# Kernel tuning notes

Measured on AMD Instinct MI355X. Metric: run time of the kernel, lower is better.

## Reference

```python
import jax, jax.numpy as jnp
import numpy as np

B = 64        # graphs per batch
N0 = 131072   # total nodes (2048 per graph)
E = 1048576   # total edges (within-graph)
H = 128       # hidden_size
C = 7         # class_num (input feature dim)
EPS = 1e-5


def setup_inputs() -> dict:
    key = jax.random.key(0)
    ks = jax.random.split(key, 16)
    n0 = N0 // B
    x = jax.random.normal(ks[0], (N0, C), dtype=jnp.float32)
    # within-graph random edges: edge e belongs to graph e // (E//B)
    g = jnp.repeat(jnp.arange(B, dtype=jnp.int32), E // B)
    row = jax.random.randint(ks[1], (E,), 0, n0, dtype=jnp.int32) + g * n0
    col = jax.random.randint(ks[2], (E,), 0, n0, dtype=jnp.int32) + g * n0
    edge_index = jnp.stack([row, col], axis=0)
    batch = jnp.repeat(jnp.arange(B, dtype=jnp.int32), n0)
    s = 0.05
    params = dict(
        Wc1=jax.random.normal(ks[3], (C, H), jnp.float32) * s,     # conv1 weight
        Wc=jax.random.normal(ks[4], (3, H, H), jnp.float32) * s,   # conv2-4 weights
        bc=jax.random.normal(ks[5], (4, H), jnp.float32) * s,      # conv biases
        Wf=jax.random.normal(ks[6], (4, H, H), jnp.float32) * s,   # fc weights
        bf=jax.random.normal(ks[7], (4, H), jnp.float32) * s,      # fc biases
        bn_g=jnp.ones((4, H), jnp.float32),                        # BN gamma
        bn_b=jnp.zeros((4, H), jnp.float32),                       # BN beta
        Ws1=jax.random.normal(ks[8], (4, H, 1), jnp.float32) * s,  # SAG GraphConv root weight
        Ws2=jax.random.normal(ks[9], (4, H, 1), jnp.float32) * s,  # SAG GraphConv neighbor weight
        bs=jax.random.normal(ks[10], (4, 1), jnp.float32) * s,     # SAG GraphConv bias
    )
    return dict(x=x, edge_index=edge_index, batch=batch, **params)


def _gcn_conv(x, W, b, row, col, m, N):
    # PyG GCNConv with self loops: out_i = sum_{j->i} h_j / sqrt(d_i d_j) + h_i / d_i + b
    h = x @ W
    deg = jax.ops.segment_sum(m, col, num_segments=N) + 1.0  # +1 for self loop
    dis = jax.lax.rsqrt(deg)
    norm = dis[row] * dis[col] * m  # masked-out edges contribute 0
    agg = jax.ops.segment_sum(h[row] * norm[:, None], col, num_segments=N)
    return agg + h * (dis * dis)[:, None] + b


def _sag_score(x, W1, W2, b, row, col, m, N):
    # GraphConv(H, 1, aggr='add'): score_i = W1^T x_i + W2^T sum_{j->i} x_j + b
    nbr = jax.ops.segment_sum(x[row] * m[:, None], col, num_segments=N)
    return (x @ W1 + nbr @ W2 + b).reshape(-1)


def _bn(x, g, b):
    mu = jnp.mean(x, axis=0)
    var = jnp.mean((x - mu) ** 2, axis=0)  # biased, matches torch BN training
    return (x - mu) * jax.lax.rsqrt(var + EPS) * g + b


def reference(x, edge_index, batch, Wc1, Wc, bc, Wf, bf, bn_g, bn_b, Ws1, Ws2, bs):
    row, col = edge_index[0], edge_index[1]
    m = jnp.ones(row.shape, x.dtype)  # edge validity mask (static-size edge list)
    n = x.shape[0] // B               # nodes per graph (equal-size graphs)
    for i in range(4):
        N = B * n
        W = Wc1 if i == 0 else Wc[i - 1]
        h = _gcn_conv(x, W, bc[i], row, col, m, N)
        h = jax.nn.relu(h @ Wf[i] + bf[i])
        h = _bn(h, bn_g[i], bn_b[i])
        # SAGPooling(ratio=0.5): per-graph top-k by GraphConv score, x *= tanh(score)
        score = _sag_score(h, Ws1[i], Ws2[i], bs[i], row, col, m, N)
        k = n // 2
        _, idx = jax.lax.top_k(score.reshape(B, n), k)  # [B, k] per-graph indices
        perm = (idx + jnp.arange(B, dtype=idx.dtype)[:, None] * n).reshape(-1)
        x = h[perm] * jnp.tanh(score[perm])[:, None]
        # re-index edges; mask edges touching removed nodes
        inv = jnp.full((N,), -1, dtype=row.dtype).at[perm].set(
            jnp.arange(B * k, dtype=row.dtype))
        nr, nc = inv[row], inv[col]
        valid = (nr >= 0) & (nc >= 0)
        m = m * valid.astype(m.dtype)
        row = jnp.where(valid, nr, 0)
        col = jnp.where(valid, nc, 0)
        n = k
    # global_mean_pool over block-structured batch -> [B, H]
    return x.reshape(B, n, -1).mean(axis=1)
```

## Files before the change

### kernel.cpp

```cpp
#include <hip/hip_runtime.h>
#include <cstdint>

#define HB 128
#define NB 64
#define NE 1048576
#define SLAB 16384
#define XP 132

typedef float v2f __attribute__((ext_vector_type(2)));

__global__ __launch_bounds__(256) void init_edges_k(const int* __restrict__ ei,
    int* __restrict__ row, int* __restrict__ col, int* __restrict__ gcnt0, int E) {
  int e = blockIdx.x * blockDim.x + threadIdx.x;
  if (e < E) { row[e] = ei[e]; col[e] = ei[E + e]; }
  if (blockIdx.x == 0 && threadIdx.x < NB) gcnt0[threadIdx.x] = SLAB;
}

__global__ __launch_bounds__(256) void conv_fc0_k(const float* __restrict__ aggx,
    const float* __restrict__ Wc1, const float* __restrict__ bc0,
    const float* __restrict__ Wf, const float* __restrict__ bf0,
    float* __restrict__ out, int N, float* __restrict__ stat) {
  __shared__ float lt[64][128];
  __shared__ float laggx[64][8];
  __shared__ float lwc1[7 * 128];
  float2 (*red)[128] = (float2(*)[128])lt;
  int tid = threadIdx.x;
  int tx = tid & 31, ty = tid >> 5;
  long rowbase = (long)blockIdx.x * 64;
  for (int i = tid; i < 7 * 32; i += 256)
    ((float4*)lwc1)[i] = ((const float4*)Wc1)[i];
  if (tid < 128) {
    int lr = tid >> 1, lq = (tid & 1) * 4;
    *(float4*)&laggx[lr][lq] = *(const float4*)(aggx + (rowbase + lr) * 8 + lq);
  }
  __syncthreads();
  float4 tacc[8];
  float4 bcv = ((const float4*)bc0)[tx];
  #pragma unroll
  for (int r = 0; r < 8; ++r) tacc[r] = bcv;
  #pragma unroll
  for (int k = 0; k < 7; ++k) {
    float4 wv = ((float4*)lwc1)[k * 32 + tx];
    #pragma unroll
    for (int r = 0; r < 8; ++r) {
      float xv = laggx[ty + 8 * r][k];
      tacc[r].x += xv * wv.x; tacc[r].y += xv * wv.y;
      tacc[r].z += xv * wv.z; tacc[r].w += xv * wv.w;
    }
  }
  #pragma unroll
  for (int r = 0; r < 8; ++r)
    *(float4*)&lt[ty + 8 * r][4 * tx] = tacc[r];
  __syncthreads();
  v2f acc2[16];
  #pragma unroll
  for (int r = 0; r < 16; ++r) acc2[r] = (v2f){0.f, 0.f};
  for (int kc = 0; kc < 16; ++kc) {
    float4 wreg[8];
    #pragma unroll
    for (int k = 0; k < 8; ++k)
      wreg[k] = *(const float4*)(Wf + (size_t)(kc * 8 + k) * HB + 4 * tx);
    #pragma unroll
    for (int kk = 0; kk < 8; kk += 4) {
      float4 xreg[8];
      #pragma unroll
      for (int r = 0; r < 8; ++r)
        xreg[r] = *(const float4*)&lt[ty + 8 * r][kc * 8 + kk];
      #pragma unroll
      for (int k2 = 0; k2 < 4; ++k2) {
        float4 wv = wreg[kk + k2];
        v2f wlo = {wv.x, wv.y}, whi = {wv.z, wv.w};
        #pragma unroll
        for (int r = 0; r < 8; ++r) {
          float xv = ((const float*)&xreg[r])[k2];
          v2f xvv = {xv, xv};
          acc2[2 * r]     += xvv * wlo;
          acc2[2 * r + 1] += xvv * whi;
        }
      }
    }
  }
  float4 bv = ((const float4*)bf0)[tx];
  float4 psum = make_float4(0.f, 0.f, 0.f, 0.f);
  float4 psq  = make_float4(0.f, 0.f, 0.f, 0.f);
  __syncthreads();
  #pragma unroll
  for (int r = 0; r < 8; ++r) {
    float4 v;
    v.x = fmaxf(acc2[2 * r].x + bv.x, 0.f);
    v.y = fmaxf(acc2[2 * r].y + bv.y, 0.f);
    v.z = fmaxf(acc2[2 * r + 1].x + bv.z, 0.f);
    v.w = fmaxf(acc2[2 * r + 1].y + bv.w, 0.f);
    psum.x += v.x; psum.y += v.y; psum.z += v.z; psum.w += v.w;
    psq.x += v.x * v.x; psq.y += v.y * v.y;
    psq.z += v.z * v.z; psq.w += v.w * v.w;
    *(float4*)(out + (size_t)(rowbase + ty + 8 * r) * HB + 4 * tx) = v;
  }
  red[ty][4 * tx + 0] = make_float2(psum.x, psq.x);
  red[ty][4 * tx + 1] = make_float2(psum.y, psq.y);
  red[ty][4 * tx + 2] = make_float2(psum.z, psq.z);
  red[ty][4 * tx + 3] = make_float2(psum.w, psq.w);
  __syncthreads();
  if (tid < 128) {
    float s = 0.f, q = 0.f;
    #pragma unroll
    for (int t = 0; t < 8; ++t) { s += red[t][tid].x; q += red[t][tid].y; }
    float* st = stat + ((blockIdx.x & 7) << 8);
    atomicAdd(&st[tid], s);
    atomicAdd(&st[128 + tid], q);
  }
}

__global__ __launch_bounds__(256) void conv_fc_k(const float* __restrict__ Ap,
    const float* __restrict__ bnsc, const int* __restrict__ sel,
    const float* __restrict__ scale, const int* __restrict__ srowA,
    const float* __restrict__ snorm2, const int* __restrict__ off,
    const int* __restrict__ offe, const float* __restrict__ dis,
    const float* __restrict__ Wc, const float* __restrict__ bc0,
    const float* __restrict__ Wf, const float* __restrict__ bf0,
    float* __restrict__ out, int N, float* __restrict__ stat) {
  __shared__ float buf[64][XP];
  float2 (*red)[128] = (float2(*)[128])buf;
  int tid = threadIdx.x;
  int tx = tid & 31, ty = tid >> 5;
  long cpx = gridDim.x >> 3;
  long bb = ((long)blockIdx.x & 7) * cpx + ((long)blockIdx.x >> 3);
  long rowbase = bb * 64;
  {
    int r = tid >> 2;
    int chq = (tid & 3) * 32;
    int node = rowbase + r;
    int e0 = off[node], e1 = offe[node];
    float dv = dis[node];
    float4 acc[8];
    float ssum;
    {
      float sc = scale[node] * dv * dv;
      ssum = sc;
      const float* xr = Ap + (size_t)sel[node] * HB + chq;
      #pragma unroll
      for (int q = 0; q < 8; ++q) {
        float4 v = *(const float4*)(xr + 4 * q);
        acc[q].x = v.x * sc; acc[q].y = v.y * sc;
        acc[q].z = v.z * sc; acc[q].w = v.w * sc;
      }
    }
    for (int j = e0; j < e1; ++j) {
      float sc = snorm2[j];
      const float* xr = Ap + (size_t)srowA[j] * HB + chq;
      ssum += sc;
      #pragma unroll
      for (int q = 0; q < 8; ++q) {
        float4 v = *(const float4*)(xr + 4 * q);
        acc[q].x += v.x * sc; acc[q].y += v.y * sc;
        acc[q].z += v.z * sc; acc[q].w += v.w * sc;
      }
    }
    #pragma unroll
    for (int q = 0; q < 8; ++q) {
      float4 a  = *(const float4*)(bnsc + chq + 4 * q);
      float4 b8 = *(const float4*)(bnsc + 128 + chq + 4 * q);
      float4 o;
      o.x = a.x * acc[q].x + b8.x * ssum;
      o.y = a.y * acc[q].y + b8.y * ssum;
      o.z = a.z * acc[q].z + b8.z * ssum;
      o.w = a.w * acc[q].w + b8.w * ssum;
      *(float4*)&buf[r][chq + 4 * q] = o;
    }
  }
  __syncthreads();
  {
    float4 bcv = ((const float4*)bc0)[tx];
    v2f acc2[16];
    #pragma unroll
    for (int r = 0; r < 8; ++r) {
      acc2[2 * r]     = (v2f){bcv.x, bcv.y};
      acc2[2 * r + 1] = (v2f){bcv.z, bcv.w};
    }
    for (int kc = 0; kc < 16; ++kc) {
      float4 wreg[8];
      #pragma unroll
      for (int k = 0; k < 8; ++k)
        wreg[k] = *(const float4*)(Wc + (size_t)(kc * 8 + k) * HB + 4 * tx);
      #pragma unroll
      for (int kk = 0; kk < 8; kk += 4) {
        float4 xreg[8];
        #pragma unroll
        for (int r = 0; r < 8; ++r)
          xreg[r] = *(const float4*)&buf[ty + 8 * r][kc * 8 + kk];
        #pragma unroll
        for (int k2 = 0; k2 < 4; ++k2) {
          float4 wv = wreg[kk + k2];
          v2f wlo = {wv.x, wv.y}, whi = {wv.z, wv.w};
          #pragma unroll
          for (int r = 0; r < 8; ++r) {
            float xv = ((const float*)&xreg[r])[k2];
            v2f xvv = {xv, xv};
            acc2[2 * r]     += xvv * wlo;
            acc2[2 * r + 1] += xvv * whi;
          }
        }
      }
    }
    __syncthreads();
    #pragma unroll
    for (int r = 0; r < 8; ++r) {
      float4 v;
      v.x = acc2[2 * r].x;     v.y = acc2[2 * r].y;
      v.z = acc2[2 * r + 1].x; v.w = acc2[2 * r + 1].y;
      *(float4*)&buf[ty + 8 * r][4 * tx] = v;
    }
  }
  __syncthreads();
  v2f acc2[16];
  #pragma unroll
  for (int r = 0; r < 16; ++r) acc2[r] = (v2f){0.f, 0.f};
  for (int kc = 0; kc < 16; ++kc) {
    float4 wreg[8];
    #pragma unroll
    for (int k = 0; k < 8; ++k)
      wreg[k] = *(const float4*)(Wf + (size_t)(kc * 8 + k) * HB + 4 * tx);
    #pragma unroll
    for (int kk = 0; kk < 8; kk += 4) {
      float4 xreg[8];
      #pragma unroll
      for (int r = 0; r < 8; ++r)
        xreg[r] = *(const float4*)&buf[ty + 8 * r][kc * 8 + kk];
      #pragma unroll
      for (int k2 = 0; k2 < 4; ++k2) {
        float4 wv = wreg[kk + k2];
        v2f wlo = {wv.x, wv.y}, whi = {wv.z, wv.w};
        #pragma unroll
        for (int r = 0; r < 8; ++r) {
          float xv = ((const float*)&xreg[r])[k2];
          v2f xvv = {xv, xv};
          acc2[2 * r]     += xvv * wlo;
          acc2[2 * r + 1] += xvv * whi;
        }
      }
    }
  }
  float4 bv = ((const float4*)bf0)[tx];
  float4 psum = make_float4(0.f, 0.f, 0.f, 0.f);
  float4 psq  = make_float4(0.f, 0.f, 0.f, 0.f);
  __syncthreads();
  #pragma unroll
  for (int r = 0; r < 8; ++r) {
    float4 v;
    v.x = fmaxf(acc2[2 * r].x + bv.x, 0.f);
    v.y = fmaxf(acc2[2 * r].y + bv.y, 0.f);
    v.z = fmaxf(acc2[2 * r + 1].x + bv.z, 0.f);
    v.w = fmaxf(acc2[2 * r + 1].y + bv.w, 0.f);
    psum.x += v.x; psum.y += v.y; psum.z += v.z; psum.w += v.w;
    psq.x += v.x * v.x; psq.y += v.y * v.y;
    psq.z += v.z * v.z; psq.w += v.w * v.w;
    *(float4*)(out + (size_t)(rowbase + ty + 8 * r) * HB + 4 * tx) = v;
  }
  red[ty][4 * tx + 0] = make_float2(psum.x, psq.x);
  red[ty][4 * tx + 1] = make_float2(psum.y, psq.y);
  red[ty][4 * tx + 2] = make_float2(psum.z, psq.z);
  red[ty][4 * tx + 3] = make_float2(psum.w, psq.w);
  __syncthreads();
  if (tid < 128) {
    float s = 0.f, q = 0.f;
    #pragma unroll
    for (int t = 0; t < 8; ++t) { s += red[t][tid].x; q += red[t][tid].y; }
    float* st = stat + (((int)blockIdx.x & 7) << 8);
    atomicAdd(&st[tid], s);
    atomicAdd(&st[128 + tid], q);
  }
}

__global__ __launch_bounds__(1024) void csr_build_k(const int* __restrict__ row,
    const int* __restrict__ col, const int* __restrict__ gcnt,
    const int* __restrict__ sel, const float* __restrict__ scale,
    float* __restrict__ dis, int* __restrict__ off, int* __restrict__ offe,
    int* __restrict__ srow, int* __restrict__ srowA,
    float* __restrict__ snorm, int n) {
  extern __shared__ int lds[];
  int* ldeg = lds;
  int* lsa  = lds + n;
  int* lsb  = lds + 2 * n;
  float* ldis = (float*)(lds + 3 * n);
  int g = blockIdx.x, tid = threadIdx.x;
  int e0 = g * SLAB, e1 = e0 + gcnt[g];
  int base = g * n;
  for (int i = tid; i < n; i += 1024) ldeg[i] = 0;
  __syncthreads();
  for (int e = e0 + tid; e < e1; e += 1024) atomicAdd(&ldeg[col[e] - base], 1);
  __syncthreads();
  for (int i = tid; i < n; i += 1024) {
    int d = ldeg[i];
    ldis[i] = rsqrtf((float)d + 1.f);
    lsa[i] = d;
  }
  __syncthreads();
  int* src = lsa; int* dst = lsb;
  for (int o = 1; o < n; o <<= 1) {
    for (int i = tid; i < n; i += 1024) dst[i] = src[i] + ((i >= o) ? src[i - o] : 0);
    __syncthreads();
    int* t = src; src = dst; dst = t;
  }
  for (int i = tid; i < n; i += 1024) {
    int d = ldeg[i];
    int ex = src[i] - d;
    off[base + i]  = e0 + ex;
    offe[base + i] = e0 + ex + d;
    ldeg[i] = ex;
    dis[base + i] = ldis[i];
  }
  __syncthreads();
  for (int e = e0 + tid; e < e1; e += 1024) {
    int r = row[e], c = col[e];
    int lc = c - base;
    int p = e0 + atomicAdd(&ldeg[lc], 1);
    srow[p] = r;
    float nm = ldis[r - base] * ldis[lc];
    if (sel) { srowA[p] = sel[r]; snorm[p] = nm * scale[r]; }
    else     { srowA[p] = r;      snorm[p] = nm; }
  }
}

__global__ __launch_bounds__(256) void agg7_k(const float* __restrict__ x,
    const int* __restrict__ srow, const float* __restrict__ snorm,
    const int* __restrict__ off, const int* __restrict__ offe,
    const float* __restrict__ dis, float* __restrict__ aggx, int N) {
  int cpx = gridDim.x >> 3;
  int b = blockIdx.x;
  int bid = (b & 7) * cpx + (b >> 3);
  int gid = bid * 256 + threadIdx.x;
  int node = gid >> 3, c = gid & 7;
  if (node >= N) return;
  float acc = 0.f;
  if (c < 7) {
    int s = off[node], e = offe[node];
    for (int j = s; j < e; ++j) acc += x[(size_t)srow[j] * 7 + c] * snorm[j];
    float d = dis[node];
    acc += x[(size_t)node * 7 + c] * d * d;
  }
  aggx[(size_t)node * 8 + c] = acc;
}

__global__ __launch_bounds__(128) void bnfin_k(const float* __restrict__ stat8,
    const float* __restrict__ g, const float* __restrict__ b,
    float* __restrict__ sc, int N) {
  int c = threadIdx.x;
  if (c < 128) {
    float s = 0.f, q = 0.f;
    #pragma unroll
    for (int sh = 0; sh < 8; ++sh) {
      s += stat8[sh * 256 + c];
      q += stat8[sh * 256 + 128 + c];
    }
    float mu = s / N;
    float var = q / N - mu * mu;
    float a = g[c] * rsqrtf(var + 1e-5f);
    sc[c] = a;
    sc[128 + c] = b[c] - mu * a;
  }
}

__global__ __launch_bounds__(256) void score_prep_k(const float* __restrict__ h,
    const float* __restrict__ sc, const float* __restrict__ w1,
    const float* __restrict__ w2, float* __restrict__ selfs,
    float* __restrict__ t2, int N) {
  int gid = blockIdx.x * blockDim.x + threadIdx.x;
  int node = gid >> 6;
  if (node >= N) return;
  int lane = gid & 63, c = lane * 2;
  float2 v = *(const float2*)(h + (size_t)node * HB + c);
  v.x = v.x * sc[c] + sc[128 + c];
  v.y = v.y * sc[c + 1] + sc[128 + c + 1];
  float s1 = v.x * w1[c] + v.y * w1[c + 1];
  float s2 = v.x * w2[c] + v.y * w2[c + 1];
  #pragma unroll
  for (int off = 32; off > 0; off >>= 1) {
    s1 += __shfl_xor(s1, off);
    s2 += __shfl_xor(s2, off);
  }
  if (lane == 0) { selfs[node] = s1; t2[node] = s2; }
}

__global__ __launch_bounds__(256) void score_k(const float* __restrict__ selfs,
    const float* __restrict__ t2, const int* __restrict__ srow,
    const int* __restrict__ off, const int* __restrict__ offe,
    const float* __restrict__ bs, float* __restrict__ score, int N) {
  int i = blockIdx.x * blockDim.x + threadIdx.x;
  if (i >= N) return;
  float s = selfs[i] + bs[0];
  int e0 = off[i], e1 = offe[i];
  for (int j = e0; j < e1; ++j) s += t2[srow[j]];
  score[i] = s;
}

__global__ __launch_bounds__(256) void rank_topk_k(const float* __restrict__ score,
    int* __restrict__ inv, int* __restrict__ sel, float* __restrict__ scale,
    int n, int k, int bpg) {
  extern __shared__ float ls[];
  int g = blockIdx.x / bpg, sub = blockIdx.x % bpg;
  int tid = threadIdx.x;
  const float* sg = score + (size_t)g * n;
  for (int i = tid; i < n; i += 256) ls[i] = sg[i];
  __syncthreads();
  int i0 = sub * 256 + tid;
  float s0 = ls[i0];
  int r0 = 0;
  for (int jb = 0; jb < n; jb += 4) {
    float4 v = *(const float4*)(ls + jb);
    r0 += (v.x > s0) || (v.x == s0 && (jb + 0) < i0);
    r0 += (v.y > s0) || (v.y == s0 && (jb + 1) < i0);
    r0 += (v.z > s0) || (v.z == s0 && (jb + 2) < i0);
    r0 += (v.w > s0) || (v.w == s0 && (jb + 3) < i0);
  }
  if (r0 < k) {
    inv[(size_t)g * n + i0] = g * k + r0;
    sel[(size_t)g * k + r0] = g * n + i0;
    scale[(size_t)g * k + r0] = tanhf(s0);
  } else inv[(size_t)g * n + i0] = -1;
}

__global__ __launch_bounds__(256) void gather_x_k(const float* __restrict__ h,
    const float* __restrict__ bnsc, const int* __restrict__ sel,
    const float* __restrict__ scale, float* __restrict__ xout, int M) {
  int gid = blockIdx.x * blockDim.x + threadIdx.x;
  int r = gid >> 5;
  if (r >= M) return;
  int ch = (gid & 31) * 4;
  int old = sel[r];
  float sc = scale[r];
  float4 v = *(const float4*)(h + (size_t)old * HB + ch);
  float4 a = *(const float4*)(bnsc + ch);
  float4 b = *(const float4*)(bnsc + 128 + ch);
  v.x = (v.x * a.x + b.x) * sc; v.y = (v.y * a.y + b.y) * sc;
  v.z = (v.z * a.z + b.z) * sc; v.w = (v.w * a.w + b.w) * sc;
  *(float4*)(xout + (size_t)r * HB + ch) = v;
}

__global__ __launch_bounds__(256) void cmp_k(const int* __restrict__ row,
    const int* __restrict__ col, const int* __restrict__ inv,
    const int* __restrict__ gcntCur, int* __restrict__ nrow,
    int* __restrict__ ncol, int* __restrict__ gcntNxt) {
  int g = blockIdx.x >> 6;
  int eloc = ((blockIdx.x & 63) << 8) + threadIdx.x;
  int cnt = gcntCur[g];
  if (((blockIdx.x & 63) << 8) >= cnt) return;
  long e = (long)g * SLAB + eloc;
  bool valid = false; int nr = 0, nc = 0;
  if (eloc < cnt) {
    nr = inv[row[e]]; nc = inv[col[e]];
    valid = (nr >= 0) && (nc >= 0);
  }
  unsigned long long mask = __ballot(valid);
  int lane = threadIdx.x & 63, wid = threadIdx.x >> 6;
  __shared__ int ws[4];
  __shared__ int base;
  if (lane == 0) ws[wid] = __popcll(mask);
  __syncthreads();
  if (threadIdx.x == 0) {
    int a = ws[0], b = ws[1], c2 = ws[2], d = ws[3];
    int tot = a + b + c2 + d;
    base = tot ? atomicAdd(&gcntNxt[g], tot) : 0;
    ws[0] = 0; ws[1] = a; ws[2] = a + b; ws[3] = a + b + c2;
  }
  __syncthreads();
  if (valid) {
    unsigned long long lt = ((unsigned long long)1 << lane) - 1;
    long o = (long)g * SLAB + base + ws[wid] + (int)__popcll(mask & lt);
    nrow[o] = nr;
    ncol[o] = nc;
  }
}

__global__ __launch_bounds__(128) void pool_k(const float* __restrict__ x,
    float* __restrict__ out, int n) {
  int g = blockIdx.x, c = threadIdx.x;
  float s = 0.f;
  for (int r = 0; r < n; ++r) s += x[((size_t)g * n + r) * HB + c];
  out[g * HB + c] = s / n;
}

extern "C" void kernel_launch(void* const* d_in, const int* in_sizes, int n_in,
                              void* d_out, int out_size, void* d_ws, size_t ws_size,
                              hipStream_t stream) {
  const float* x_in = (const float*)d_in[0];
  const int*   ei   = (const int*)d_in[1];
  const float* Wc1  = (const float*)d_in[3];
  const float* Wc   = (const float*)d_in[4];
  const float* bc   = (const float*)d_in[5];
  const float* Wf   = (const float*)d_in[6];
  const float* bf   = (const float*)d_in[7];
  const float* bng  = (const float*)d_in[8];
  const float* bnb  = (const float*)d_in[9];
  const float* Ws1  = (const float*)d_in[10];
  const float* Ws2  = (const float*)d_in[11];
  const float* bs   = (const float*)d_in[12];

  const int N0 = 131072, E = NE;
  char* p = (char*)d_ws;
  auto alloc = [&](size_t bytes) -> char* {
    char* r = p; p += (bytes + 255) & ~(size_t)255; return r;
  };
  float* A    = (float*)alloc((size_t)N0 * HB * 4);
  float* Bb   = (float*)alloc((size_t)N0 * HB * 4);
  float* Cc   = (float*)alloc((size_t)(N0 / 2) * HB * 4);
  float* aggx = (float*)alloc((size_t)N0 * 8 * 4);
  int*   rowA = (int*)alloc((size_t)E * 4);
  int*   colA = (int*)alloc((size_t)E * 4);
  int*   rowB = (int*)alloc((size_t)E * 4);
  int*   colB = (int*)alloc((size_t)E * 4);
  int*   srowA= (int*)alloc((size_t)E * 4);
  float* dis  = (float*)alloc((size_t)N0 * 4);
  float* selfs= (float*)alloc((size_t)N0 * 4);
  float* t2v  = (float*)alloc((size_t)N0 * 4);
  float* score= (float*)alloc((size_t)N0 * 4);
  int*   inv  = (int*)alloc((size_t)N0 * 4);
  int*   off  = (int*)alloc((size_t)N0 * 4);
  int*   offe = (int*)alloc((size_t)N0 * 4);
  int*   sel  = (int*)alloc((size_t)(N0 / 2) * 4);
  float* scale= (float*)alloc((size_t)(N0 / 2) * 4);
  int*   gcntL= (int*)alloc(4 * NB * 4);
  float* stat8= (float*)alloc(4 * 8 * 256 * 4);
  float* bnsc = (float*)alloc(256 * 4);

  hipMemsetAsync(stat8, 0, 4 * 8 * 256 * 4, stream);
  hipMemsetAsync(gcntL, 0, 4 * NB * 4, stream);

  init_edges_k<<<E / 256, 256, 0, stream>>>(ei, rowA, colA, gcntL, E);

  int* rowCur = rowA; int* colCur = colA;
  int* rowNxt = rowB; int* colNxt = colB;

  int n = 2048;
  for (int i = 0; i < 4; ++i) {
    int N = NB * n, khalf = n >> 1;
    float* statL = stat8 + (size_t)i * 8 * 256;
    const float* Xin  = (i == 2) ? Bb : A;
    float*       Xout = (i == 0 || i == 2) ? A : Bb;
    int*   srow  = rowNxt;
    float* snorm = (float*)colNxt;
    csr_build_k<<<NB, 1024, (size_t)16 * n, stream>>>(
        rowCur, colCur, gcntL + i * NB, (i == 0) ? nullptr : sel,
        (i == 0) ? nullptr : scale, dis, off, offe, srow, srowA, snorm, n);
    if (i == 0) {
      agg7_k<<<N / 32, 256, 0, stream>>>(x_in, srow, snorm, off, offe, dis, aggx, N);
      conv_fc0_k<<<N / 64, 256, 0, stream>>>(aggx, Wc1, bc, Wf, bf, Xout, N, statL);
    } else {
      conv_fc_k<<<N / 64, 256, 0, stream>>>(
          Xin, bnsc, sel, scale, srowA, snorm, off, offe, dis,
          Wc + (size_t)(i - 1) * HB * HB, bc + (size_t)i * HB,
          Wf + (size_t)i * HB * HB, bf + (size_t)i * HB, Xout, N, statL);
    }
    bnfin_k<<<1, 128, 0, stream>>>(statL, bng + (size_t)i * HB, bnb + (size_t)i * HB, bnsc, N);
    score_prep_k<<<N / 4, 256, 0, stream>>>(
        Xout, bnsc, Ws1 + (size_t)i * HB, Ws2 + (size_t)i * HB, selfs, t2v, N);
    score_k<<<(N + 255) / 256, 256, 0, stream>>>(
        selfs, t2v, srow, off, offe, bs + i, score, N);
    int bpg = n / 256;
    rank_topk_k<<<NB * bpg, 256, (size_t)n * 4, stream>>>(
        score, inv, sel, scale, n, khalf, bpg);
    if (i < 3) {
      cmp_k<<<NB * 64, 256, 0, stream>>>(rowCur, colCur, inv, gcntL + i * NB,
                                         rowNxt, colNxt, gcntL + (i + 1) * NB);
      int* t;
      t = rowCur; rowCur = rowNxt; rowNxt = t;
      t = colCur; colCur = colNxt; colNxt = t;
    } else {
      gather_x_k<<<(NB * khalf) / 8, 256, 0, stream>>>(
          Xout, bnsc, sel, scale, Cc, NB * khalf);
    }
    n = khalf;
  }
  pool_k<<<NB, 128, 0, stream>>>(Cc, (float*)d_out, n);
}
```

Measured before the change: 601.6 us.

## Split fused gather-aggregate and dense FC kernel into two separate kernels

Splits conv_fc_k into gatherx_k, which does the irregular neighbor gather and normalization and writes the aggregated features to a new xagg buffer, and fc2_k, which loads xagg and runs the two dense matmuls plus the BN statistics. The aim is to stop the latency-bound gather from stalling the compute-heavy GEMM in the same block, so each kernel can reach its own occupancy and scheduling. The cost is an extra global round trip of an N×128 float buffer and one more launch per layer.

```diff
diff --git a/kernel.cpp b/kernel.cpp
--- a/kernel.cpp
+++ b/kernel.cpp
@@ -111,11 +111,60 @@
   }
 }
 
-__global__ __launch_bounds__(256) void conv_fc_k(const float* __restrict__ Ap,
+__global__ __launch_bounds__(256) void gatherx_k(const float* __restrict__ Ap,
     const float* __restrict__ bnsc, const int* __restrict__ sel,
     const float* __restrict__ scale, const int* __restrict__ srowA,
     const float* __restrict__ snorm2, const int* __restrict__ off,
     const int* __restrict__ offe, const float* __restrict__ dis,
+    float* __restrict__ xagg, int N) {
+  int cpx = gridDim.x >> 3;
+  int b = blockIdx.x;
+  int bid = (b & 7) * cpx + (b >> 3);
+  int gid = bid * 256 + threadIdx.x;
+  int node = gid >> 2;
+  if (node >= N) return;
+  int chq = (gid & 3) * 32;
+  int e0 = off[node], e1 = offe[node];
+  float dv = dis[node];
+  float4 acc[8];
+  float ssum;
+  {
+    float sc = scale[node] * dv * dv;
+    ssum = sc;
+    const float* xr = Ap + (size_t)sel[node] * HB + chq;
+    #pragma unroll
+    for (int q = 0; q < 8; ++q) {
+      float4 v = *(const float4*)(xr + 4 * q);
+      acc[q].x = v.x * sc; acc[q].y = v.y * sc;
+      acc[q].z = v.z * sc; acc[q].w = v.w * sc;
+    }
+  }
+  for (int j = e0; j < e1; ++j) {
+    float sc = snorm2[j];
+    const float* xr = Ap + (size_t)srowA[j] * HB + chq;
+    ssum += sc;
+    #pragma unroll
+    for (int q = 0; q < 8; ++q) {
+      float4 v = *(const float4*)(xr + 4 * q);
+      acc[q].x += v.x * sc; acc[q].y += v.y * sc;
+      acc[q].z += v.z * sc; acc[q].w += v.w * sc;
+    }
+  }
+  float* outp = xagg + (size_t)node * HB + chq;
+  #pragma unroll
+  for (int q = 0; q < 8; ++q) {
+    float4 a  = *(const float4*)(bnsc + chq + 4 * q);
+    float4 b8 = *(const float4*)(bnsc + 128 + chq + 4 * q);
+    float4 o;
+    o.x = a.x * acc[q].x + b8.x * ssum;
+    o.y = a.y * acc[q].y + b8.y * ssum;
+    o.z = a.z * acc[q].z + b8.z * ssum;
+    o.w = a.w * acc[q].w + b8.w * ssum;
+    *(float4*)(outp + 4 * q) = o;
+  }
+}
+
+__global__ __launch_bounds__(256) void fc2_k(const float* __restrict__ xagg,
     const float* __restrict__ Wc, const float* __restrict__ bc0,
     const float* __restrict__ Wf, const float* __restrict__ bf0,
     float* __restrict__ out, int N, float* __restrict__ stat) {
@@ -123,50 +172,14 @@
   float2 (*red)[128] = (float2(*)[128])buf;
   int tid = threadIdx.x;
   int tx = tid & 31, ty = tid >> 5;
-  long cpx = gridDim.x >> 3;
-  long bb = ((long)blockIdx.x & 7) * cpx + ((long)blockIdx.x >> 3);
-  long rowbase = bb * 64;
+  long rowbase = (long)blockIdx.x * 64;
   {
     int r = tid >> 2;
     int chq = (tid & 3) * 32;
-    int node = rowbase + r;
-    int e0 = off[node], e1 = offe[node];
-    float dv = dis[node];
-    float4 acc[8];
-    float ssum;
-    {
-      float sc = scale[node] * dv * dv;
-      ssum = sc;
-      const float* xr = Ap + (size_t)sel[node] * HB + chq;
-      #pragma unroll
-      for (int q = 0; q < 8; ++q) {
-        float4 v = *(const float4*)(xr + 4 * q);
-        acc[q].x = v.x * sc; acc[q].y = v.y * sc;
-        acc[q].z = v.z * sc; acc[q].w = v.w * sc;
-      }
-    }
-    for (int j = e0; j < e1; ++j) {
-      float sc = snorm2[j];
-      const float* xr = Ap + (size_t)srowA[j] * HB + chq;
-      ssum += sc;
-      #pragma unroll
-      for (int q = 0; q < 8; ++q) {
-        float4 v = *(const float4*)(xr + 4 * q);
-        acc[q].x += v.x * sc; acc[q].y += v.y * sc;
-        acc[q].z += v.z * sc; acc[q].w += v.w * sc;
-      }
-    }
-    #pragma unroll
-    for (int q = 0; q < 8; ++q) {
-      float4 a  = *(const float4*)(bnsc + chq + 4 * q);
-      float4 b8 = *(const float4*)(bnsc + 128 + chq + 4 * q);
-      float4 o;
-      o.x = a.x * acc[q].x + b8.x * ssum;
-      o.y = a.y * acc[q].y + b8.y * ssum;
-      o.z = a.z * acc[q].z + b8.z * ssum;
-      o.w = a.w * acc[q].w + b8.w * ssum;
-      *(float4*)&buf[r][chq + 4 * q] = o;
-    }
+    const float* xr = xagg + (rowbase + r) * HB + chq;
+    #pragma unroll
+    for (int q = 0; q < 8; ++q)
+      *(float4*)&buf[r][chq + 4 * q] = *(const float4*)(xr + 4 * q);
   }
   __syncthreads();
   {
@@ -503,6 +516,7 @@
   float* A    = (float*)alloc((size_t)N0 * HB * 4);
   float* Bb   = (float*)alloc((size_t)N0 * HB * 4);
   float* Cc   = (float*)alloc((size_t)(N0 / 2) * HB * 4);
+  float* xagg = (float*)alloc((size_t)(N0 / 2) * HB * 4);
   float* aggx = (float*)alloc((size_t)N0 * 8 * 4);
   int*   rowA = (int*)alloc((size_t)E * 4);
   int*   colA = (int*)alloc((size_t)E * 4);
@@ -545,9 +559,10 @@
       agg7_k<<<N / 32, 256, 0, stream>>>(x_in, srow, snorm, off, offe, dis, aggx, N);
       conv_fc0_k<<<N / 64, 256, 0, stream>>>(aggx, Wc1, bc, Wf, bf, Xout, N, statL);
     } else {
-      conv_fc_k<<<N / 64, 256, 0, stream>>>(
-          Xin, bnsc, sel, scale, srowA, snorm, off, offe, dis,
-          Wc + (size_t)(i - 1) * HB * HB, bc + (size_t)i * HB,
+      gatherx_k<<<N / 64, 256, 0, stream>>>(
+          Xin, bnsc, sel, scale, srowA, snorm, off, offe, dis, xagg, N);
+      fc2_k<<<N / 64, 256, 0, stream>>>(
+          xagg, Wc + (size_t)(i - 1) * HB * HB, bc + (size_t)i * HB,
           Wf + (size_t)i * HB * HB, bf + (size_t)i * HB, Xout, N, statL);
     }
     bnfin_k<<<1, 128, 0, stream>>>(statL, bng + (size_t)i * HB, bnb + (size_t)i * HB, bnsc, N);
```

Measured after the change: 645.9 us. 7.4% more time.
